# Kernel tuning notes

Measured on AMD Instinct MI355X. Metric: run time of the kernel, lower is better.

Reference implementation:

```python
import jax, jax.numpy as jnp
import numpy as np

NMUL = 1
NEARZERO = 1e-5
ROUTING_LEN = 15
N_DYN = 3
N_STATIC = 13  # layout includes parRT, parAC (present in STATIC_PARAM_NAMES but unused in the step)


def _descale(x, lb, ub):
    return lb + x * (ub - lb)


def setup_inputs() -> dict:
    key = jax.random.key(0)
    k1, k2, k3 = jax.random.split(key, 3)
    T, G = 365, 50000
    u = jax.random.uniform(k1, (T, G, 3), dtype=jnp.float32)
    prcp = u[..., 0] * 10.0                 # mm/day
    tmean = (u[..., 1] - 0.3) * 20.0        # degC, roughly [-6, 14] so snow branch is exercised
    pet = u[..., 2] * 5.0                   # mm/day
    forcing = jnp.stack([prcp, tmean, pet], axis=-1)
    dyn_raw = jax.random.uniform(k2, (T, G, N_DYN * NMUL), dtype=jnp.float32)
    static_raw = jax.random.uniform(k3, (G, N_STATIC * NMUL + 2), dtype=jnp.float32)
    return {"forcing": forcing, "dyn_raw": dyn_raw, "static_raw": static_raw}


def _hbv_forward(forcing, dyn_raw, static_raw):
    T, G, _ = forcing.shape
    dt = forcing.dtype
    # --- descale dynamic params (per-timestep): parBETA, parK0, parBETAET ---
    dyn = dyn_raw.reshape(T, G, N_DYN, NMUL)
    parBETA = _descale(dyn[:, :, 0], 1.0, 6.0)
    parK0 = _descale(dyn[:, :, 1], 0.05, 0.9)
    parBETAET = _descale(dyn[:, :, 2], 0.3, 5.0)
    # --- descale static params ---
    st = static_raw[:, :N_STATIC * NMUL].reshape(G, N_STATIC, NMUL)
    parFC = _descale(st[:, 0], 50.0, 1000.0)
    parK1 = _descale(st[:, 1], 0.01, 0.5)
    parK2 = _descale(st[:, 2], 0.001, 0.2)
    parLP = _descale(st[:, 3], 0.2, 1.0)
    parPERC = _descale(st[:, 4], 0.0, 10.0)
    parUZL = _descale(st[:, 5], 0.0, 100.0)
    parTT = _descale(st[:, 6], -2.5, 2.5)
    parCFMAX = _descale(st[:, 7], 0.5, 10.0)
    parCFR = _descale(st[:, 8], 0.0, 0.1)
    parCWH = _descale(st[:, 9], 0.0, 0.2)
    parC = _descale(st[:, 10], 0.0, 1.0)
    rout = static_raw[:, N_STATIC * NMUL:]
    rout_a = _descale(rout[:, 0], 0.0, 2.9)
    rout_b = _descale(rout[:, 1], 0.0, 6.5)

    Pm = jnp.broadcast_to(forcing[..., 0:1], (T, G, NMUL))
    Tm = jnp.broadcast_to(forcing[..., 1:2], (T, G, NMUL))
    PETm = jnp.broadcast_to(forcing[..., 2:3], (T, G, NMUL))

    def step(carry, xs):
        SNOWPACK, MELTWATER, SM, SUZ, SLZ = carry
        PRECIP, TEMP, PET, pBETA, pK0, pBETAET = xs
        is_rain = (TEMP >= parTT).astype(dt)
        RAIN = PRECIP * is_rain
        SNOW = PRECIP * (1.0 - is_rain)
        SNOWPACK = SNOWPACK + SNOW
        melt = jnp.minimum(jnp.maximum(parCFMAX * (TEMP - parTT), 0.0), SNOWPACK)
        MELTWATER = MELTWATER + melt
        SNOWPACK = SNOWPACK - melt
        refreezing = jnp.minimum(jnp.maximum(parCFR * parCFMAX * (parTT - TEMP), 0.0), MELTWATER)
        SNOWPACK = SNOWPACK + refreezing
        MELTWATER = MELTWATER - refreezing
        tosoil = jnp.maximum(MELTWATER - parCWH * SNOWPACK, 0.0)
        MELTWATER = MELTWATER - tosoil
        soil_wetness = jnp.clip((SM / parFC) ** pBETA, 0.0, 1.0)
        recharge = (RAIN + tosoil) * soil_wetness
        SM = SM + RAIN + tosoil - recharge
        excess = jnp.maximum(SM - parFC, 0.0)
        SM = SM - excess
        evapfactor = jnp.clip((SM / (parLP * parFC)) ** pBETAET, 0.0, 1.0)
        ETact = jnp.minimum(SM, PET * evapfactor)
        SM = jnp.maximum(SM - ETact, NEARZERO)
        capillary = jnp.minimum(SLZ, parC * SLZ * (1.0 - jnp.minimum(SM / parFC, 1.0)))
        SM = jnp.maximum(SM + capillary, NEARZERO)
        SLZ = jnp.maximum(SLZ - capillary, NEARZERO)
        SUZ = SUZ + recharge + excess
        PERC = jnp.minimum(SUZ, parPERC)
        SUZ = SUZ - PERC
        Q0 = pK0 * jnp.maximum(SUZ - parUZL, 0.0)
        SUZ = SUZ - Q0
        Q1 = parK1 * SUZ
        SUZ = SUZ - Q1
        SLZ = jnp.maximum(SLZ + PERC, 0.0)
        Q2 = parK2 * SLZ
        SLZ = SLZ - Q2
        return (SNOWPACK, MELTWATER, SM, SUZ, SLZ), Q0 + Q1 + Q2

    init = tuple(jnp.full((G, NMUL), 0.001, dtype=dt) for _ in range(5))
    _, Qall = jax.lax.scan(step, init, (Pm, Tm, PETm, parBETA, parK0, parBETAET))
    Qsim = Qall.mean(axis=-1)  # [T, G]: average over nmul components

    # --- gamma unit-hydrograph routing (hydroDL UH_gamma + causal conv, lenF = 15) ---
    aa = jax.nn.relu(rout_a) + 0.1      # shape param, [G]
    theta = jax.nn.relu(rout_b) + 0.5   # scale param, [G]
    t = jnp.arange(0.5, ROUTING_LEN, dtype=dt)[:, None]  # [15, 1] midpoints
    w = (t ** (aa - 1.0)) * jnp.exp(-t / theta) / (jnp.exp(jax.lax.lgamma(aa)) * theta ** aa)
    w = w / w.sum(axis=0)  # [15, G], normalized UH weights
    Qpad = jnp.pad(Qsim, ((ROUTING_LEN - 1, 0), (0, 0)))
    # causal conv: Qrout[t] = sum_k w[k] * Qsim[t-k]; fixed 15-tap loop
    Qrout = sum(w[k] * jax.lax.dynamic_slice_in_dim(Qpad, ROUTING_LEN - 1 - k, T, axis=0)
                for k in range(ROUTING_LEN))
    return Qrout  # streamflow [T, G]


def reference(forcing, dyn_raw, static_raw):
    return _hbv_forward(forcing, dyn_raw, static_raw)
```

## Files before the change

kernel.cpp:

```cpp
#include <hip/hip_runtime.h>

#define NEARZERO 1e-5f
#define RLEN 15
#define LOG2E 1.4426950408889634f

struct __attribute__((packed, aligned(4))) F3 { float x, y, z; };
static __device__ __forceinline__ F3 ldo(const char* base, unsigned voff) {
    return *reinterpret_cast<const F3*>(base + voff);
}

struct Par { float FC, invFC, invLPFC, K1, K2, PERC, UZL, TT, CFMAX, CFRC, CWH, C; };

__device__ __forceinline__ void ab_step(
    const F3& f, const F3& d3, const Par& pr,
    float& SP, float& MW, float& SM, float& SLZ,
    float cs, float& rxP, float& k0P)
{
    const float pBETA   = fmaf(d3.x, 5.0f, 1.0f);
    const float pBETAET = fmaf(d3.z, 4.7f, 0.3f);
    const float dT   = f.y - pr.TT;
    const float RAIN = (dT >= 0.0f) ? f.x : 0.0f;
    SP += f.x - RAIN;
    const float melt = __builtin_amdgcn_fmed3f(pr.CFMAX * dT, 0.0f, SP);
    MW += melt;  SP -= melt;
    const float refr = __builtin_amdgcn_fmed3f(pr.CFRC * (0.0f - dT), 0.0f, MW);
    SP += refr;  MW -= refr;
    const float tosoil = fmaxf(fmaf(-pr.CWH, SP, MW), 0.0f);
    MW -= tosoil;
    const float sw = fminf(exp2f(pBETA * __log2f(SM * pr.invFC)), 1.0f);
    const float rt = RAIN + tosoil;
    const float rc = rt * sw;
    SM = fmaf(rt, 1.0f - sw, SM);
    const float ex = fmaxf(SM - pr.FC, 0.0f);
    SM = fminf(SM, pr.FC);
    const float ef = fminf(exp2f(pBETAET * __log2f(SM * pr.invLPFC)), 1.0f);
    SM = fmaxf(SM - f.z * ef, NEARZERO);
    const float cap = cs * (1.0f - fminf(SM * pr.invFC, 1.0f));
    SM  = fmaxf(SM + cap, NEARZERO);
    SLZ = fmaxf(SLZ - cap, NEARZERO);
    rxP = rc + ex;
    k0P = fmaf(d3.y, 0.85f, 0.05f);
}

template<int PH>
__device__ __forceinline__ void fused_iter(
    const F3 f, const F3 d3, const Par& pr,
    float& SP, float& MW, float& SM, float& SUZ, float& SLZ,
    float& rxP, float& k0P,
    float (&acc)[RLEN], const float (&w)[RLEN],
    float* outp, bool guard)
{
    const float t1 = __log2f(SM * pr.invFC);
    const float dT   = f.y - pr.TT;
    const float RAIN = (dT >= 0.0f) ? f.x : 0.0f;
    SP += f.x - RAIN;
    const float melt = __builtin_amdgcn_fmed3f(pr.CFMAX * dT, 0.0f, SP);
    MW += melt;  SP -= melt;
    const float refr = __builtin_amdgcn_fmed3f(pr.CFRC * (0.0f - dT), 0.0f, MW);
    SP += refr;  MW -= refr;
    const float tosoil = fmaxf(fmaf(-pr.CWH, SP, MW), 0.0f);
    MW -= tosoil;
    SUZ += rxP;
    const float PERCv = fminf(SUZ, pr.PERC);
    SUZ -= PERCv;
    const float Q0 = k0P * fmaxf(SUZ - pr.UZL, 0.0f);
    SUZ -= Q0;
    const float Q1 = pr.K1 * SUZ;
    SUZ -= Q1;
    const float pBETA = fmaf(d3.x, 5.0f, 1.0f);
    const float sw = fminf(exp2f(pBETA * t1), 1.0f);
    const float rt = RAIN + tosoil;
    SLZ += PERCv;
    const float Q2 = pr.K2 * SLZ;
    SLZ -= Q2;
    const float Qs = Q0 + Q1 + Q2;
    const float cs = pr.C * SLZ;
    const float rc = rt * sw;
    SM = fmaf(rt, 1.0f - sw, SM);
    const float ex = fmaxf(SM - pr.FC, 0.0f);
    SM = fminf(SM, pr.FC);
    const float t2 = __log2f(SM * pr.invLPFC);
    const float qr = fmaf(w[0], Qs, acc[PH]);
    acc[PH] = 0.0f;
#pragma unroll
    for (int k = 1; k < RLEN; ++k) {
        const int j = (PH + k) % RLEN;
        acc[j] = fmaf(w[k], Qs, acc[j]);
    }
    if (guard) __builtin_nontemporal_store(qr, outp);
    const float pBETAET = fmaf(d3.z, 4.7f, 0.3f);
    const float ef = fminf(exp2f(pBETAET * t2), 1.0f);
    SM = fmaxf(SM - f.z * ef, NEARZERO);
    const float cap = cs * (1.0f - fminf(SM * pr.invFC, 1.0f));
    SM  = fmaxf(SM + cap, NEARZERO);
    SLZ = fmaxf(SLZ - cap, NEARZERO);
    rxP = rc + ex;
    k0P = fmaf(d3.y, 0.85f, 0.05f);
}

template<int PH>
__device__ __forceinline__ void finish_step(
    const Par& pr, float& SUZ, float& SLZ, float rxP, float k0P,
    float (&acc)[RLEN], const float (&w)[RLEN], float* outp, bool guard)
{
    SUZ += rxP;
    const float PERCv = fminf(SUZ, pr.PERC);
    SUZ -= PERCv;
    const float Q0 = k0P * fmaxf(SUZ - pr.UZL, 0.0f);
    SUZ -= Q0;
    const float Q1 = pr.K1 * SUZ;
    SUZ -= Q1;
    SLZ += PERCv;
    const float Q2 = pr.K2 * SLZ;
    SLZ -= Q2;
    const float Qs = Q0 + Q1 + Q2;
    const float qr = fmaf(w[0], Qs, acc[PH]);
    if (guard) __builtin_nontemporal_store(qr, outp);
}

__global__ __launch_bounds__(256, 1)
void hbv_kernel(const float* __restrict__ forcing,
                const float* __restrict__ dynr,
                const float* __restrict__ statr,
                float* __restrict__ out,
                int G)
{
    const int g  = blockIdx.x * 256 + threadIdx.x;
    const int gc = (g < G) ? g : (G - 1);
    const bool guard = (g < G);

    const float* sp = statr + (size_t)gc * 15;
    Par pr;
    pr.FC    = fmaf(sp[0], 950.0f, 50.0f);
    pr.K1    = fmaf(sp[1], 0.49f, 0.01f);
    pr.K2    = fmaf(sp[2], 0.199f, 0.001f);
    const float parLP = fmaf(sp[3], 0.8f, 0.2f);
    pr.PERC  = sp[4] * 10.0f;
    pr.UZL   = sp[5] * 100.0f;
    pr.TT    = fmaf(sp[6], 5.0f, -2.5f);
    pr.CFMAX = fmaf(sp[7], 9.5f, 0.5f);
    pr.CFRC  = (sp[8] * 0.1f) * pr.CFMAX;
    pr.CWH   = sp[9] * 0.2f;
    pr.C     = sp[10];
    const float rout_a = sp[13] * 2.9f;
    const float rout_b = sp[14] * 6.5f;
    pr.invFC   = 1.0f / pr.FC;
    pr.invLPFC = 1.0f / (parLP * pr.FC);

    const float aa    = fmaxf(rout_a, 0.0f) + 0.1f;
    const float theta = fmaxf(rout_b, 0.0f) + 0.5f;
    const float am1   = aa - 1.0f;
    const float nitl2 = -LOG2E / theta;
    float w[RLEN];
    float wsum = 0.0f;
#pragma unroll
    for (int k = 0; k < RLEN; ++k) {
        const float tk = (float)k + 0.5f;
        w[k] = exp2f(am1 * __log2f(tk) + tk * nitl2);
        wsum += w[k];
    }
    const float winv = 1.0f / wsum;
#pragma unroll
    for (int k = 0; k < RLEN; ++k) w[k] *= winv;

    float SP_ = 0.001f, MW = 0.001f, SM = 0.001f, SUZ = 0.001f, SLZ = 0.001f;
    float acc[RLEN];
#pragma unroll
    for (int k = 0; k < RLEN; ++k) acc[k] = 0.0f;
    float rxP = 0.0f, k0P = 0.0f;

    const char* fbase = (const char*)forcing;
    const char* dbase = (const char*)dynr;
    char*       obase = (char*)out;
    const unsigned G12 = (unsigned)G * 12u;
    const unsigned G4  = (unsigned)G * 4u;
    unsigned vRun = (unsigned)gc * 12u;
    unsigned vO   = (unsigned)g  * 4u;

    F3 bF[5], bD[5];
#pragma unroll
    for (int r = 0; r < 5; ++r) {
        bF[r] = ldo(fbase, vRun); bD[r] = ldo(dbase, vRun);
        vRun += G12;
    }

    {
        const float cs0 = pr.C * SLZ;
        const F3 f_ = bF[0], d_ = bD[0];
        bF[0] = ldo(fbase, vRun); bD[0] = ldo(dbase, vRun);
        vRun += G12;
        __builtin_amdgcn_sched_barrier(0x7);
        ab_step(f_, d_, pr, SP_, MW, SM, SLZ, cs0, rxP, k0P);
    }

#define ITER(MM, VOFF) do { \
    constexpr int PH_ = (MM) % RLEN; \
    constexpr int S_  = ((MM) + 1) % 5; \
    const F3 f_ = bF[S_], d_ = bD[S_]; \
    bF[S_] = ldo(fbase, (VOFF)); bD[S_] = ldo(dbase, (VOFF)); \
    __builtin_amdgcn_sched_barrier(0x7); \
    fused_iter<PH_>(f_, d_, pr, SP_, MW, SM, SUZ, SLZ, rxP, k0P, acc, w, \
                    (float*)(obase + vO), guard); \
    vO += G4; \
} while (0)

#define ITERADV(MM) do { ITER(MM, vRun); vRun += G12; } while (0)

#define ITER_NL(MM) do { \
    constexpr int PH_ = (MM) % RLEN; \
    constexpr int S_  = ((MM) + 1) % 5; \
    const F3 f_ = bF[S_], d_ = bD[S_]; \
    fused_iter<PH_>(f_, d_, pr, SP_, MW, SM, SUZ, SLZ, rxP, k0P, acc, w, \
                    (float*)(obase + vO), guard); \
    vO += G4; \
} while (0)

    for (int i = 0; i < 23; ++i) {
        ITERADV(0);  ITERADV(1);  ITERADV(2);  ITERADV(3);  ITERADV(4);
        ITERADV(5);  ITERADV(6);  ITERADV(7);  ITERADV(8);  ITERADV(9);
        ITERADV(10); ITERADV(11); ITERADV(12); ITERADV(13); ITERADV(14);
    }
    ITERADV(0);  ITERADV(1);  ITERADV(2);  ITERADV(3);  ITERADV(4);
    ITERADV(5);  ITERADV(6);  ITERADV(7);  ITERADV(8);  ITERADV(9);
    ITERADV(10); ITERADV(11); ITERADV(12); ITERADV(13);
    ITER(14, (unsigned)gc * 12u + 364u * G12);
    ITER_NL(0); ITER_NL(1); ITER_NL(2); ITER_NL(3);
    finish_step<4>(pr, SUZ, SLZ, rxP, k0P, acc, w, (float*)(obase + vO), guard);
#undef ITER_NL
#undef ITERADV
#undef ITER
}

extern "C" void kernel_launch(void* const* d_in, const int* in_sizes, int n_in,
                              void* d_out, int out_size, void* d_ws, size_t ws_size,
                              hipStream_t stream) {
    const float* forcing = (const float*)d_in[0];
    const float* dynr    = (const float*)d_in[1];
    const float* statr   = (const float*)d_in[2];
    float* out = (float*)d_out;

    const int G = in_sizes[2] / 15;
    const int block = 256;
    const int grid  = (G + block - 1) / block;
    hbv_kernel<<<grid, block, 0, stream>>>(forcing, dynr, statr, out, G);
}
```

Before: 97.81 us.

## Split HBV recurrence and routing FIR into producer and consumer waves via LDS

```diff
diff --git a/kernel.cpp b/kernel.cpp
--- a/kernel.cpp
+++ b/kernel.cpp
@@ -11,13 +11,12 @@
 
 struct Par { float FC, invFC, invLPFC, K1, K2, PERC, UZL, TT, CFMAX, CFRC, CWH, C; };
 
-__device__ __forceinline__ void ab_step(
-    const F3& f, const F3& d3, const Par& pr,
+__device__ __forceinline__ void ab_step0(
+    const F3 f, const F3 d3, const Par& pr,
     float& SP, float& MW, float& SM, float& SLZ,
-    float cs, float& rxP, float& k0P)
+    float& rxP, float& k0P)
 {
-    const float pBETA   = fmaf(d3.x, 5.0f, 1.0f);
-    const float pBETAET = fmaf(d3.z, 4.7f, 0.3f);
+    const float cs = pr.C * SLZ;
     const float dT   = f.y - pr.TT;
     const float RAIN = (dT >= 0.0f) ? f.x : 0.0f;
     SP += f.x - RAIN;
@@ -27,13 +26,13 @@
     SP += refr;  MW -= refr;
     const float tosoil = fmaxf(fmaf(-pr.CWH, SP, MW), 0.0f);
     MW -= tosoil;
-    const float sw = fminf(exp2f(pBETA * __log2f(SM * pr.invFC)), 1.0f);
+    const float sw = fminf(exp2f(fmaf(d3.x, 5.0f, 1.0f) * __log2f(SM * pr.invFC)), 1.0f);
     const float rt = RAIN + tosoil;
     const float rc = rt * sw;
     SM = fmaf(rt, 1.0f - sw, SM);
     const float ex = fmaxf(SM - pr.FC, 0.0f);
     SM = fminf(SM, pr.FC);
-    const float ef = fminf(exp2f(pBETAET * __log2f(SM * pr.invLPFC)), 1.0f);
+    const float ef = fminf(exp2f(fmaf(d3.z, 4.7f, 0.3f) * __log2f(SM * pr.invLPFC)), 1.0f);
     SM = fmaxf(SM - f.z * ef, NEARZERO);
     const float cap = cs * (1.0f - fminf(SM * pr.invFC, 1.0f));
     SM  = fmaxf(SM + cap, NEARZERO);
@@ -42,13 +41,12 @@
     k0P = fmaf(d3.y, 0.85f, 0.05f);
 }
 
-template<int PH>
-__device__ __forceinline__ void fused_iter(
+template<int I, int B>
+__device__ __forceinline__ void fused0(
     const F3 f, const F3 d3, const Par& pr,
     float& SP, float& MW, float& SM, float& SUZ, float& SLZ,
     float& rxP, float& k0P,
-    float (&acc)[RLEN], const float (&w)[RLEN],
-    float* outp, bool guard)
+    float (*qbuf)[RLEN][64], int lane)
 {
     const float t1 = __log2f(SM * pr.invFC);
     const float dT   = f.y - pr.TT;
@@ -67,29 +65,20 @@
     SUZ -= Q0;
     const float Q1 = pr.K1 * SUZ;
     SUZ -= Q1;
-    const float pBETA = fmaf(d3.x, 5.0f, 1.0f);
-    const float sw = fminf(exp2f(pBETA * t1), 1.0f);
+    const float sw = fminf(exp2f(fmaf(d3.x, 5.0f, 1.0f) * t1), 1.0f);
     const float rt = RAIN + tosoil;
     SLZ += PERCv;
     const float Q2 = pr.K2 * SLZ;
     SLZ -= Q2;
     const float Qs = Q0 + Q1 + Q2;
     const float cs = pr.C * SLZ;
+    qbuf[B][I][lane] = Qs;
     const float rc = rt * sw;
     SM = fmaf(rt, 1.0f - sw, SM);
     const float ex = fmaxf(SM - pr.FC, 0.0f);
     SM = fminf(SM, pr.FC);
     const float t2 = __log2f(SM * pr.invLPFC);
-    const float qr = fmaf(w[0], Qs, acc[PH]);
-    acc[PH] = 0.0f;
-#pragma unroll
-    for (int k = 1; k < RLEN; ++k) {
-        const int j = (PH + k) % RLEN;
-        acc[j] = fmaf(w[k], Qs, acc[j]);
-    }
-    if (guard) __builtin_nontemporal_store(qr, outp);
-    const float pBETAET = fmaf(d3.z, 4.7f, 0.3f);
-    const float ef = fminf(exp2f(pBETAET * t2), 1.0f);
+    const float ef = fminf(exp2f(fmaf(d3.z, 4.7f, 0.3f) * t2), 1.0f);
     SM = fmaxf(SM - f.z * ef, NEARZERO);
     const float cap = cs * (1.0f - fminf(SM * pr.invFC, 1.0f));
     SM  = fmaxf(SM + cap, NEARZERO);
@@ -98,137 +87,153 @@
     k0P = fmaf(d3.y, 0.85f, 0.05f);
 }
 
-template<int PH>
-__device__ __forceinline__ void finish_step(
-    const Par& pr, float& SUZ, float& SLZ, float rxP, float k0P,
-    float (&acc)[RLEN], const float (&w)[RLEN], float* outp, bool guard)
-{
-    SUZ += rxP;
-    const float PERCv = fminf(SUZ, pr.PERC);
-    SUZ -= PERCv;
-    const float Q0 = k0P * fmaxf(SUZ - pr.UZL, 0.0f);
-    SUZ -= Q0;
-    const float Q1 = pr.K1 * SUZ;
-    SUZ -= Q1;
-    SLZ += PERCv;
-    const float Q2 = pr.K2 * SLZ;
-    SLZ -= Q2;
-    const float Qs = Q0 + Q1 + Q2;
-    const float qr = fmaf(w[0], Qs, acc[PH]);
-    if (guard) __builtin_nontemporal_store(qr, outp);
-}
-
-__global__ __launch_bounds__(256, 1)
+__global__ __launch_bounds__(128, 1)
 void hbv_kernel(const float* __restrict__ forcing,
                 const float* __restrict__ dynr,
                 const float* __restrict__ statr,
                 float* __restrict__ out,
                 int G)
 {
-    const int g  = blockIdx.x * 256 + threadIdx.x;
+    __shared__ float qbuf[2][RLEN][64];
+
+    const int lane = threadIdx.x & 63;
+    const int wave = threadIdx.x >> 6;
+    const int g  = blockIdx.x * 64 + lane;
     const int gc = (g < G) ? g : (G - 1);
-    const bool guard = (g < G);
-
-    const float* sp = statr + (size_t)gc * 15;
-    Par pr;
-    pr.FC    = fmaf(sp[0], 950.0f, 50.0f);
-    pr.K1    = fmaf(sp[1], 0.49f, 0.01f);
-    pr.K2    = fmaf(sp[2], 0.199f, 0.001f);
-    const float parLP = fmaf(sp[3], 0.8f, 0.2f);
-    pr.PERC  = sp[4] * 10.0f;
-    pr.UZL   = sp[5] * 100.0f;
-    pr.TT    = fmaf(sp[6], 5.0f, -2.5f);
-    pr.CFMAX = fmaf(sp[7], 9.5f, 0.5f);
-    pr.CFRC  = (sp[8] * 0.1f) * pr.CFMAX;
-    pr.CWH   = sp[9] * 0.2f;
-    pr.C     = sp[10];
-    const float rout_a = sp[13] * 2.9f;
-    const float rout_b = sp[14] * 6.5f;
-    pr.invFC   = 1.0f / pr.FC;
-    pr.invLPFC = 1.0f / (parLP * pr.FC);
-
-    const float aa    = fmaxf(rout_a, 0.0f) + 0.1f;
-    const float theta = fmaxf(rout_b, 0.0f) + 0.5f;
-    const float am1   = aa - 1.0f;
-    const float nitl2 = -LOG2E / theta;
-    float w[RLEN];
-    float wsum = 0.0f;
-#pragma unroll
-    for (int k = 0; k < RLEN; ++k) {
-        const float tk = (float)k + 0.5f;
-        w[k] = exp2f(am1 * __log2f(tk) + tk * nitl2);
-        wsum += w[k];
+
+    if (wave == 0) {
+        const float* sp = statr + (size_t)gc * 15;
+        Par pr;
+        pr.FC    = fmaf(sp[0], 950.0f, 50.0f);
+        pr.K1    = fmaf(sp[1], 0.49f, 0.01f);
+        pr.K2    = fmaf(sp[2], 0.199f, 0.001f);
+        const float parLP = fmaf(sp[3], 0.8f, 0.2f);
+        pr.PERC  = sp[4] * 10.0f;
+        pr.UZL   = sp[5] * 100.0f;
+        pr.TT    = fmaf(sp[6], 5.0f, -2.5f);
+        pr.CFMAX = fmaf(sp[7], 9.5f, 0.5f);
+        pr.CFRC  = (sp[8] * 0.1f) * pr.CFMAX;
+        pr.CWH   = sp[9] * 0.2f;
+        pr.C     = sp[10];
+        pr.invFC   = 1.0f / pr.FC;
+        pr.invLPFC = 1.0f / (parLP * pr.FC);
+
+        float SP_ = 0.001f, MW = 0.001f, SM = 0.001f, SUZ = 0.001f, SLZ = 0.001f;
+        float rxP = 0.0f, k0P = 0.0f;
+
+        const char* fbase = (const char*)forcing;
+        const char* dbase = (const char*)dynr;
+        const unsigned G12 = (unsigned)G * 12u;
+        unsigned vRun = (unsigned)gc * 12u;
+
+        F3 bF[5], bD[5];
+#pragma unroll
+        for (int r = 0; r < 5; ++r) {
+            bF[r] = ldo(fbase, vRun); bD[r] = ldo(dbase, vRun);
+            vRun += G12;
+        }
+
+        {
+            const F3 f_ = bF[0], d_ = bD[0];
+            bF[0] = ldo(fbase, vRun); bD[0] = ldo(dbase, vRun);
+            vRun += G12;
+            __builtin_amdgcn_sched_barrier(0x7);
+            ab_step0(f_, d_, pr, SP_, MW, SM, SLZ, rxP, k0P);
+        }
+
+#define W0(I, B, VOFF, DOLOAD) do { \
+        constexpr int S_ = ((I) + 1) % 5; \
+        const F3 f_ = bF[S_], d_ = bD[S_]; \
+        if (DOLOAD) { bF[S_] = ldo(fbase, (VOFF)); bD[S_] = ldo(dbase, (VOFF)); } \
+        __builtin_amdgcn_sched_barrier(0x7); \
+        fused0<(I), (B)>(f_, d_, pr, SP_, MW, SM, SUZ, SLZ, rxP, k0P, qbuf, lane); \
+} while (0)
+#define W0ADV(I, B) do { W0(I, B, vRun, true); vRun += G12; } while (0)
+#define W0G15(B) do { \
+        W0ADV(0,B);  W0ADV(1,B);  W0ADV(2,B);  W0ADV(3,B);  W0ADV(4,B); \
+        W0ADV(5,B);  W0ADV(6,B);  W0ADV(7,B);  W0ADV(8,B);  W0ADV(9,B); \
+        W0ADV(10,B); W0ADV(11,B); W0ADV(12,B); W0ADV(13,B); W0ADV(14,B); \
+} while (0)
+
+        for (int jj = 0; jj < 11; ++jj) {
+            W0G15(0);
+            __syncthreads();
+            W0G15(1);
+            __syncthreads();
+        }
+        W0G15(0);
+        __syncthreads();
+        W0ADV(0,1);  W0ADV(1,1);  W0ADV(2,1);  W0ADV(3,1);  W0ADV(4,1);
+        W0ADV(5,1);  W0ADV(6,1);  W0ADV(7,1);  W0ADV(8,1);  W0ADV(9,1);
+        W0ADV(10,1); W0ADV(11,1); W0ADV(12,1); W0ADV(13,1);
+        W0(14, 1, (unsigned)gc * 12u + 364u * G12, true);
+        __syncthreads();
+        W0(0,0,0u,false); W0(1,0,0u,false); W0(2,0,0u,false);
+        W0(3,0,0u,false); W0(4,0,0u,false);
+        __syncthreads();
+        return;
+#undef W0G15
+#undef W0ADV
+#undef W0
     }
-    const float winv = 1.0f / wsum;
-#pragma unroll
-    for (int k = 0; k < RLEN; ++k) w[k] *= winv;
-
-    float SP_ = 0.001f, MW = 0.001f, SM = 0.001f, SUZ = 0.001f, SLZ = 0.001f;
-    float acc[RLEN];
-#pragma unroll
-    for (int k = 0; k < RLEN; ++k) acc[k] = 0.0f;
-    float rxP = 0.0f, k0P = 0.0f;
-
-    const char* fbase = (const char*)forcing;
-    const char* dbase = (const char*)dynr;
-    char*       obase = (char*)out;
-    const unsigned G12 = (unsigned)G * 12u;
-    const unsigned G4  = (unsigned)G * 4u;
-    unsigned vRun = (unsigned)gc * 12u;
-    unsigned vO   = (unsigned)g  * 4u;
-
-    F3 bF[5], bD[5];
-#pragma unroll
-    for (int r = 0; r < 5; ++r) {
-        bF[r] = ldo(fbase, vRun); bD[r] = ldo(dbase, vRun);
-        vRun += G12;
+
+    {
+        const float* sp = statr + (size_t)gc * 15;
+        const float rout_a = sp[13] * 2.9f;
+        const float rout_b = sp[14] * 6.5f;
+        const float aa    = fmaxf(rout_a, 0.0f) + 0.1f;
+        const float theta = fmaxf(rout_b, 0.0f) + 0.5f;
+        const float am1   = aa - 1.0f;
+        const float nitl2 = -LOG2E / theta;
+        float w[RLEN];
+        float wsum = 0.0f;
+#pragma unroll
+        for (int k = 0; k < RLEN; ++k) {
+            const float tk = (float)k + 0.5f;
+            w[k] = exp2f(am1 * __log2f(tk) + tk * nitl2);
+            wsum += w[k];
+        }
+        const float winv = 1.0f / wsum;
+#pragma unroll
+        for (int k = 0; k < RLEN; ++k) w[k] *= winv;
+
+        float acc[RLEN];
+#pragma unroll
+        for (int k = 0; k < RLEN; ++k) acc[k] = 0.0f;
+
+        char* obase = (char*)out;
+        const unsigned G4 = (unsigned)G * 4u;
+        unsigned vO = (unsigned)g * 4u;
+        const bool guard = (g < G);
+
+#define FIRG(B, CNT) do { \
+        _Pragma("unroll") \
+        for (int i = 0; i < (CNT); ++i) { \
+            const float Qs = qbuf[B][i][lane]; \
+            const float qr = fmaf(w[0], Qs, acc[i]); \
+            acc[i] = 0.0f; \
+            _Pragma("unroll") \
+            for (int k = 1; k < RLEN; ++k) \
+                acc[(i + k) % RLEN] = fmaf(w[k], Qs, acc[(i + k) % RLEN]); \
+            if (guard) __builtin_nontemporal_store(qr, (float*)(obase + vO)); \
+            vO += G4; \
+        } \
+} while (0)
+
+        for (int jj = 0; jj < 11; ++jj) {
+            __syncthreads();
+            FIRG(0, RLEN);
+            __syncthreads();
+            FIRG(1, RLEN);
+        }
+        __syncthreads();
+        FIRG(0, RLEN);
+        __syncthreads();
+        FIRG(1, RLEN);
+        __syncthreads();
+        FIRG(0, 5);
+#undef FIRG
     }
-
-    {
-        const float cs0 = pr.C * SLZ;
-        const F3 f_ = bF[0], d_ = bD[0];
-        bF[0] = ldo(fbase, vRun); bD[0] = ldo(dbase, vRun);
-        vRun += G12;
-        __builtin_amdgcn_sched_barrier(0x7);
-        ab_step(f_, d_, pr, SP_, MW, SM, SLZ, cs0, rxP, k0P);
-    }
-
-#define ITER(MM, VOFF) do { \
-    constexpr int PH_ = (MM) % RLEN; \
-    constexpr int S_  = ((MM) + 1) % 5; \
-    const F3 f_ = bF[S_], d_ = bD[S_]; \
-    bF[S_] = ldo(fbase, (VOFF)); bD[S_] = ldo(dbase, (VOFF)); \
-    __builtin_amdgcn_sched_barrier(0x7); \
-    fused_iter<PH_>(f_, d_, pr, SP_, MW, SM, SUZ, SLZ, rxP, k0P, acc, w, \
-                    (float*)(obase + vO), guard); \
-    vO += G4; \
-} while (0)
-
-#define ITERADV(MM) do { ITER(MM, vRun); vRun += G12; } while (0)
-
-#define ITER_NL(MM) do { \
-    constexpr int PH_ = (MM) % RLEN; \
-    constexpr int S_  = ((MM) + 1) % 5; \
-    const F3 f_ = bF[S_], d_ = bD[S_]; \
-    fused_iter<PH_>(f_, d_, pr, SP_, MW, SM, SUZ, SLZ, rxP, k0P, acc, w, \
-                    (float*)(obase + vO), guard); \
-    vO += G4; \
-} while (0)
-
-    for (int i = 0; i < 23; ++i) {
-        ITERADV(0);  ITERADV(1);  ITERADV(2);  ITERADV(3);  ITERADV(4);
-        ITERADV(5);  ITERADV(6);  ITERADV(7);  ITERADV(8);  ITERADV(9);
-        ITERADV(10); ITERADV(11); ITERADV(12); ITERADV(13); ITERADV(14);
-    }
-    ITERADV(0);  ITERADV(1);  ITERADV(2);  ITERADV(3);  ITERADV(4);
-    ITERADV(5);  ITERADV(6);  ITERADV(7);  ITERADV(8);  ITERADV(9);
-    ITERADV(10); ITERADV(11); ITERADV(12); ITERADV(13);
-    ITER(14, (unsigned)gc * 12u + 364u * G12);
-    ITER_NL(0); ITER_NL(1); ITER_NL(2); ITER_NL(3);
-    finish_step<4>(pr, SUZ, SLZ, rxP, k0P, acc, w, (float*)(obase + vO), guard);
-#undef ITER_NL
-#undef ITERADV
-#undef ITER
 }
 
 extern "C" void kernel_launch(void* const* d_in, const int* in_sizes, int n_in,
@@ -240,7 +245,7 @@
     float* out = (float*)d_out;
 
     const int G = in_sizes[2] / 15;
-    const int block = 256;
-    const int grid  = (G + block - 1) / block;
+    const int block = 128;
+    const int grid  = (G + 63) / 64;
     hbv_kernel<<<grid, block, 0, stream>>>(forcing, dynr, statr, out, G);
 }
```

New measurement: 124.1 us. 1.27x slower.
